# Performance work log

Hardware: AMD Instinct MI355X
Metric: run time of the kernel (lower is better)

Reference implementation:

```python
import jax, jax.numpy as jnp
import numpy as np

B, T, D = 1024, 20, 50          # batch sessions, seq len (hardcoded 20), emb dim (hardcoded 50)
S1S2 = 50 * 20                  # sample1 * sample2 friend nodes (GAT src)
DEG = 50                        # avg in-degree per dst node
E = B * DEG
NUM_USERS, NUM_ITEMS = 100000, 50000


def _lstm(x, W_ih, W_hh, b_ih, b_hh):
    """PyTorch-style LSTM (gate order i,f,g,o). x: [N,T,D] -> hs: [T,N,D]."""
    N = x.shape[0]
    h0 = jnp.zeros((N, x.shape[-1]), x.dtype)
    def step(carry, xt):
        h, c = carry
        gates = xt @ W_ih.T + h @ W_hh.T + b_ih + b_hh
        i, f, g, o = jnp.split(gates, 4, axis=-1)
        c = jax.nn.sigmoid(f) * c + jax.nn.sigmoid(i) * jnp.tanh(g)
        h = jax.nn.sigmoid(o) * jnp.tanh(c)
        return (h, c), h
    (_, _), hs = jax.lax.scan(step, (h0, h0), jnp.swapaxes(x, 0, 1))
    return hs


def _gat(feat_src, feat_dst, edge_src, edge_dst, fc_W, fc_b):
    """u_dot_v -> edge_softmax (per dst) -> u_mul_e_sum -> relu(fc)."""
    n_dst = feat_dst.shape[0]
    src_e = feat_src[edge_src]                           # [E, D] gather
    score = jnp.sum(src_e * feat_dst[edge_dst], axis=-1) # [E] u_dot_v
    m = jax.ops.segment_max(score, edge_dst, num_segments=n_dst)
    ex = jnp.exp(score - m[edge_dst])
    den = jax.ops.segment_sum(ex, edge_dst, num_segments=n_dst)
    w = ex / den[edge_dst]                               # edge_softmax
    agg = jax.ops.segment_sum(w[:, None] * src_e, edge_dst, num_segments=n_dst)
    return jax.nn.relu(agg @ fc_W.T + fc_b)


def setup_inputs() -> dict:
    key = jax.random.key(0)
    ks = jax.random.split(key, 16)
    input_session = jax.random.randint(ks[0], (B, T), 0, NUM_ITEMS, dtype=jnp.int32)
    support_nodes_layer1 = jax.random.randint(ks[1], (S1S2,), 0, NUM_USERS, dtype=jnp.int32)
    support_sessions_layer1 = jax.random.randint(ks[2], (S1S2, T), 0, NUM_ITEMS, dtype=jnp.int32)
    edge_src = jax.random.randint(ks[3], (E,), 0, S1S2, dtype=jnp.int32)
    edge_dst = jnp.repeat(jnp.arange(B, dtype=jnp.int32), DEG)  # every dst has DEG edges
    s = 0.05
    user_emb = jax.random.normal(ks[4], (NUM_USERS, D), jnp.float32) * s
    item_emb = (jax.random.normal(ks[5], (NUM_ITEMS, D), jnp.float32) * s).at[0].set(0.0)  # padding_idx=0
    W_ih = jax.random.normal(ks[6], (4 * D, D), jnp.float32) * s
    W_hh = jax.random.normal(ks[7], (4 * D, D), jnp.float32) * s
    b_ih = jax.random.normal(ks[8], (4 * D,), jnp.float32) * s
    b_hh = jax.random.normal(ks[9], (4 * D,), jnp.float32) * s
    W1 = jax.random.normal(ks[10], (D, 2 * D), jnp.float32) * s
    fc_W = jax.random.normal(ks[11], (D, D), jnp.float32) * s
    fc_b = jax.random.normal(ks[12], (D,), jnp.float32) * s
    W2 = jax.random.normal(ks[13], (D, 3 * D), jnp.float32) * s
    return {"input_session": input_session, "support_nodes_layer1": support_nodes_layer1,
            "support_sessions_layer1": support_sessions_layer1, "edge_src": edge_src,
            "edge_dst": edge_dst, "user_emb": user_emb, "item_emb": item_emb,
            "W_ih": W_ih, "W_hh": W_hh, "b_ih": b_ih, "b_hh": b_hh,
            "W1": W1, "fc_W": fc_W, "fc_b": fc_b, "W2": W2}


def reference(input_session, support_nodes_layer1, support_sessions_layer1, edge_src, edge_dst,
              user_emb, item_emb, W_ih, W_hh, b_ih, b_hh, W1, fc_W, fc_b, W2):
    # current-user short-term: LSTM over session item embeddings, take last hidden
    output = _lstm(item_emb[input_session], W_ih, W_hh, b_ih, b_hh)[-1]        # [B, D]
    # friends long-term (user emb) + short-term (LSTM over friend sessions, step 0 as in source)
    long_term1 = user_emb[support_nodes_layer1]                                 # [S1S2, D]
    short_term1 = _lstm(item_emb[support_sessions_layer1], W_ih, W_hh, b_ih, b_hh)[0]  # [S1S2, D]
    ls1 = jax.nn.relu(jnp.concatenate([long_term1, short_term1], axis=-1) @ W1.T)      # [S1S2, D]
    # GAT: gather -> per-dst edge softmax -> scatter weighted sum
    gat_out = _gat(ls1, output, edge_src, edge_dst, fc_W, fc_b)                 # [B, D]
    feat = jnp.concatenate([output, gat_out], axis=-1)                          # [B, 2D]
    sr = jnp.concatenate([output, feat], axis=-1) @ W2.T                        # [B, D]
    logits = sr @ item_emb[1:].T                                                # [B, NUM_ITEMS-1]
    return logits
```

## Files before the change

kernel.cpp:

```cpp
#include <hip/hip_runtime.h>
#include <math.h>

#define D 50
#define T 20
#define BATCH 1024
#define S1S2 1000
#define DEG 50
#define NITEMS 50000
#define NLOGITS 49999
#define KPAD 64
#define NIPAD 50048
#define LROW 520
#define CHUNKS 98
#define CHUNKS_PAD 104
#define PREP_BLKS ((NIPAD * (KPAD / 2) + 255) / 256)

using bf16x8 = __attribute__((ext_vector_type(8))) __bf16;
using f32x4  = __attribute__((ext_vector_type(4))) float;

__device__ __forceinline__ float sigf(float x) { return 1.0f / (1.0f + expf(-x)); }

__device__ __forceinline__ unsigned short f2bf(float f) {
    unsigned u = __builtin_bit_cast(unsigned, f);
    u = (u + 0x7FFFu + ((u >> 16) & 1u)) >> 16;
    return (unsigned short)u;
}

__global__ __launch_bounds__(256) void fused_front_kernel(
    const int* __restrict__ sess,
    const int* __restrict__ nodes,
    const int* __restrict__ fsess,
    const float* __restrict__ user_emb,
    const float* __restrict__ item_emb,
    const float* __restrict__ W_ih,
    const float* __restrict__ W_hh,
    const float* __restrict__ b_ih,
    const float* __restrict__ b_hh,
    const float* __restrict__ W1,
    float* __restrict__ out_h,
    float* __restrict__ ls1,
    unsigned* __restrict__ item_u)
{
    const int blk = blockIdx.x;
    const int t = threadIdx.x;

    if (blk < BATCH) {
        const int b = blk;
        __shared__ float x_s[D];
        __shared__ float h_s[D];
        __shared__ float g_s[4 * D];
        __shared__ int idx_s[T];

        if (t < T) idx_s[t] = sess[b * T + t];

        float wih[D], whh[D];
        float bias = 0.f;
        if (t < 4 * D) {
            #pragma unroll
            for (int k = 0; k < D; ++k) {
                wih[k] = W_ih[t * D + k];
                whh[k] = W_hh[t * D + k];
            }
            bias = b_ih[t] + b_hh[t];
        }
        float c = 0.f;
        if (t < D) h_s[t] = 0.f;
        __syncthreads();
        if (t < D) x_s[t] = item_emb[(size_t)idx_s[0] * D + t];
        __syncthreads();

        for (int step = 0; step < T; ++step) {
            float xn = 0.f;
            if (t < D && step + 1 < T)
                xn = item_emb[(size_t)idx_s[step + 1] * D + t];
            if (t < 4 * D) {
                float g = bias;
                #pragma unroll
                for (int k = 0; k < D; ++k)
                    g += wih[k] * x_s[k] + whh[k] * h_s[k];
                g_s[t] = g;
            }
            __syncthreads();
            if (t < D) {
                float ig = sigf(g_s[t]);
                float fg = sigf(g_s[D + t]);
                float gg = tanhf(g_s[2 * D + t]);
                float og = sigf(g_s[3 * D + t]);
                c = fg * c + ig * gg;
                h_s[t] = og * tanhf(c);
                if (step + 1 < T) x_s[t] = xn;
            }
            __syncthreads();
        }
        if (t < D) out_h[b * D + t] = h_s[t];
    } else if (blk < BATCH + S1S2) {
        const int s = blk - BATCH;
        __shared__ float fx_s[D];
        __shared__ float fh_s[D];
        __shared__ float fg_s[4 * D];

        if (t < D) fx_s[t] = item_emb[(size_t)fsess[s * T] * D + t];
        __syncthreads();
        if (t < 4 * D) {
            float g = b_ih[t] + b_hh[t];
            #pragma unroll
            for (int k = 0; k < D; ++k) g += W_ih[t * D + k] * fx_s[k];
            fg_s[t] = g;
        }
        __syncthreads();
        if (t < D) {
            float ig = sigf(fg_s[t]);
            float gg = tanhf(fg_s[2 * D + t]);
            float og = sigf(fg_s[3 * D + t]);
            float c1 = ig * gg;
            fh_s[t] = og * tanhf(c1);
        }
        __syncthreads();
        if (t < D) {
            const int node = nodes[s];
            const float* ue = user_emb + (size_t)node * D;
            const float* w1r = W1 + t * 2 * D;
            float acc = 0.f;
            #pragma unroll
            for (int k = 0; k < D; ++k) acc += ue[k] * w1r[k];
            #pragma unroll
            for (int k = 0; k < D; ++k) acc += fh_s[k] * w1r[D + k];
            ls1[s * D + t] = fmaxf(acc, 0.f);
        }
    } else {
        const int idx = (blk - BATCH - S1S2) * 256 + t;
        if (idx >= NIPAD * (KPAD / 2)) return;
        const int r = idx >> 5, c2 = idx & 31;
        const int c0 = c2 * 2, c1 = c0 + 1;
        float f0 = 0.f, f1 = 0.f;
        if (r < NLOGITS) {
            const float* row = item_emb + (size_t)(1 + r) * D;
            if (c0 < D) f0 = row[c0];
            if (c1 < D) f1 = row[c1];
        }
        item_u[idx] = (unsigned)f2bf(f0) | ((unsigned)f2bf(f1) << 16);
    }
}

__global__ __launch_bounds__(64) void gat_sr_kernel(
    const float* __restrict__ out_h,
    const float* __restrict__ ls1,
    const int* __restrict__ edge_src,
    const float* __restrict__ fc_W,
    const float* __restrict__ fc_b,
    const float* __restrict__ W2,
    unsigned* __restrict__ sr_u)
{
    const int b = blockIdx.x;
    const int l = threadIdx.x;
    __shared__ float q[D];
    __shared__ int srcs[DEG];
    __shared__ float w_s[DEG];
    __shared__ float a_s[D];
    __shared__ float g_s[D];
    __shared__ float srow_s[KPAD];

    srow_s[l] = 0.f;
    if (l < D) q[l] = out_h[b * D + l];
    if (l < DEG) srcs[l] = edge_src[b * DEG + l];
    __syncthreads();

    float sc = -INFINITY;
    if (l < DEG) {
        const float* row = ls1 + (size_t)srcs[l] * D;
        float s = 0.f;
        #pragma unroll
        for (int k = 0; k < D; ++k) s += row[k] * q[k];
        sc = s;
    }
    float m = sc;
    #pragma unroll
    for (int off = 32; off; off >>= 1) m = fmaxf(m, __shfl_xor(m, off));
    float ex = (l < DEG) ? expf(sc - m) : 0.f;
    float den = ex;
    #pragma unroll
    for (int off = 32; off; off >>= 1) den += __shfl_xor(den, off);
    if (l < DEG) w_s[l] = ex / den;
    __syncthreads();

    if (l < D) {
        float a = 0.f;
        #pragma unroll
        for (int j = 0; j < DEG; ++j) a += w_s[j] * ls1[(size_t)srcs[j] * D + l];
        a_s[l] = a;
    }
    __syncthreads();
    if (l < D) {
        float g = fc_b[l];
        #pragma unroll
        for (int k = 0; k < D; ++k) g += a_s[k] * fc_W[l * D + k];
        g_s[l] = fmaxf(g, 0.f);
    }
    __syncthreads();
    if (l < D) {
        const float* w2r = W2 + l * 3 * D;
        float v = 0.f;
        #pragma unroll
        for (int k = 0; k < D; ++k) v += q[k] * (w2r[k] + w2r[D + k]);
        #pragma unroll
        for (int k = 0; k < D; ++k) v += g_s[k] * w2r[2 * D + k];
        srow_s[l] = v;
    }
    __syncthreads();
    if (l < KPAD / 2) {
        unsigned u = (unsigned)f2bf(srow_s[2 * l]) |
                     ((unsigned)f2bf(srow_s[2 * l + 1]) << 16);
        sr_u[b * (KPAD / 2) + l] = u;
    }
}

__global__ __launch_bounds__(256) void logits_mfma_kernel(
    const unsigned short* __restrict__ sr_bf,
    const unsigned short* __restrict__ item_bf,
    float* __restrict__ out)
{
    const int n = blockIdx.x;
    const int slab = n / CHUNKS_PAD;
    const int j = n - slab * CHUNKS_PAD;
    const int chunk = (j & 7) * 13 + (j >> 3);
    if (chunk >= CHUNKS) return;

    const int t = threadIdx.x;
    const int lane = t & 63;
    const int wave = t >> 6;
    const int r16 = lane & 15;
    const int g   = lane >> 4;
    const int b0 = slab * 16;
    const int ibase = chunk * 512;
    const int i0w = ibase + wave * 128;

    __shared__ float ls[16 * LROW];

    const unsigned short* bp = sr_bf + (size_t)(b0 + r16) * KPAD + g * 8;
    bf16x8 bv0 = *(const bf16x8*)(bp);
    bf16x8 bv1 = *(const bf16x8*)(bp + 32);

    #pragma unroll
    for (int m = 0; m < 8; ++m) {
        int irow = i0w + m * 16 + r16;
        const unsigned short* ap =
            item_bf + (size_t)(irow < NIPAD ? irow : NIPAD - 1) * KPAD + g * 8;
        bf16x8 av0 = *(const bf16x8*)(ap);
        bf16x8 av1 = *(const bf16x8*)(ap + 32);
        f32x4 acc = {0.f, 0.f, 0.f, 0.f};
        acc = __builtin_amdgcn_mfma_f32_16x16x32_bf16(av0, bv0, acc, 0, 0, 0);
        acc = __builtin_amdgcn_mfma_f32_16x16x32_bf16(av1, bv1, acc, 0, 0, 0);
        *(f32x4*)&ls[r16 * LROW + wave * 128 + m * 16 + g * 4] = acc;
    }
    __syncthreads();

    #pragma unroll
    for (int pass = 0; pass < 4; ++pass) {
        const int row = wave * 4 + pass;
        float* orow = out + (size_t)(b0 + row) * NLOGITS + ibase;
        #pragma unroll
        for (int it2 = 0; it2 < 2; ++it2) {
            const int c = lane * 4 + it2 * 256;
            const int i = ibase + c;
            f32x4 v = *(const f32x4*)&ls[row * LROW + c];
            if (i + 3 < NLOGITS) {
                *(float4*)(orow + c) = make_float4(v[0], v[1], v[2], v[3]);
            } else {
                #pragma unroll
                for (int r = 0; r < 4; ++r)
                    if (i + r < NLOGITS) orow[c + r] = v[r];
            }
        }
    }
}

extern "C" void kernel_launch(void* const* d_in, const int* in_sizes, int n_in,
                              void* d_out, int out_size, void* d_ws, size_t ws_size,
                              hipStream_t stream) {
    const int*   sess      = (const int*)d_in[0];
    const int*   nodes     = (const int*)d_in[1];
    const int*   fsess     = (const int*)d_in[2];
    const int*   edge_src  = (const int*)d_in[3];
    const float* user_emb  = (const float*)d_in[5];
    const float* item_emb  = (const float*)d_in[6];
    const float* W_ih      = (const float*)d_in[7];
    const float* W_hh      = (const float*)d_in[8];
    const float* b_ih      = (const float*)d_in[9];
    const float* b_hh      = (const float*)d_in[10];
    const float* W1        = (const float*)d_in[11];
    const float* fc_W      = (const float*)d_in[12];
    const float* fc_b      = (const float*)d_in[13];
    const float* W2        = (const float*)d_in[14];
    float* out = (float*)d_out;

    char* ws = (char*)d_ws;
    float*    out_h  = (float*)(ws);
    float*    ls1    = (float*)(ws + 204800);
    unsigned* sr_u   = (unsigned*)(ws + 404800);
    unsigned* item_u = (unsigned*)(ws + 535872);

    hipLaunchKernelGGL(fused_front_kernel,
                       dim3(BATCH + S1S2 + PREP_BLKS), dim3(256), 0, stream,
                       sess, nodes, fsess, user_emb, item_emb,
                       W_ih, W_hh, b_ih, b_hh, W1, out_h, ls1, item_u);
    hipLaunchKernelGGL(gat_sr_kernel, dim3(BATCH), dim3(64), 0, stream,
                       out_h, ls1, edge_src, fc_W, fc_b, W2, sr_u);
    hipLaunchKernelGGL(logits_mfma_kernel,
                       dim3((BATCH / 16) * CHUNKS_PAD), dim3(256), 0, stream,
                       (const unsigned short*)sr_u, (const unsigned short*)item_u, out);
}
```

Baseline: 111.9 us.

## Retile logits GEMM to 64-batch by 64-item tiles with scalar stores

The logits kernel now gives each block a 64 batch rows by 64 items tile instead of 16 rows by 512 items. Each wave loads one item fragment and loops over four batch sub-tiles. The store phase writes one float per lane per row instead of float4 vectors. This changes the reuse balance between item rows and batch rows and the grid shape, and it pads the item count to 50176, which also grows the prep work. The trade is more blocks and narrower, possibly less efficient global stores against the ~200MB output write.

```diff
diff --git a/kernel.cpp b/kernel.cpp
--- a/kernel.cpp
+++ b/kernel.cpp
@@ -9,10 +9,11 @@
 #define NITEMS 50000
 #define NLOGITS 49999
 #define KPAD 64
-#define NIPAD 50048
-#define LROW 520
-#define CHUNKS 98
-#define CHUNKS_PAD 104
+#define SLAB 64
+#define CHW 64
+#define NCHN 784
+#define NIPAD (NCHN * CHW)
+#define LROWI 66
 #define PREP_BLKS ((NIPAD * (KPAD / 2) + 255) / 256)
 
 using bf16x8 = __attribute__((ext_vector_type(8))) __bf16;
@@ -220,57 +221,44 @@
     float* __restrict__ out)
 {
     const int n = blockIdx.x;
-    const int slab = n / CHUNKS_PAD;
-    const int j = n - slab * CHUNKS_PAD;
-    const int chunk = (j & 7) * 13 + (j >> 3);
-    if (chunk >= CHUNKS) return;
+    const int slab = n / NCHN;
+    const int j = n - slab * NCHN;
+    const int chunk = (j & 7) * 98 + (j >> 3);
 
     const int t = threadIdx.x;
     const int lane = t & 63;
     const int wave = t >> 6;
     const int r16 = lane & 15;
     const int g   = lane >> 4;
-    const int b0 = slab * 16;
-    const int ibase = chunk * 512;
-    const int i0w = ibase + wave * 128;
-
-    __shared__ float ls[16 * LROW];
-
-    const unsigned short* bp = sr_bf + (size_t)(b0 + r16) * KPAD + g * 8;
-    bf16x8 bv0 = *(const bf16x8*)(bp);
-    bf16x8 bv1 = *(const bf16x8*)(bp + 32);
-
-    #pragma unroll
-    for (int m = 0; m < 8; ++m) {
-        int irow = i0w + m * 16 + r16;
-        const unsigned short* ap =
-            item_bf + (size_t)(irow < NIPAD ? irow : NIPAD - 1) * KPAD + g * 8;
-        bf16x8 av0 = *(const bf16x8*)(ap);
-        bf16x8 av1 = *(const bf16x8*)(ap + 32);
+    const int b0 = slab * SLAB;
+    const int ibase = chunk * CHW;
+
+    __shared__ float ls[SLAB * LROWI];
+
+    const unsigned short* ap =
+        item_bf + (size_t)(ibase + wave * 16 + r16) * KPAD + g * 8;
+    bf16x8 av0 = *(const bf16x8*)(ap);
+    bf16x8 av1 = *(const bf16x8*)(ap + 32);
+
+    #pragma unroll
+    for (int bt = 0; bt < 4; ++bt) {
+        const unsigned short* bp = sr_bf + (size_t)(b0 + bt * 16 + r16) * KPAD + g * 8;
+        bf16x8 bv0 = *(const bf16x8*)(bp);
+        bf16x8 bv1 = *(const bf16x8*)(bp + 32);
         f32x4 acc = {0.f, 0.f, 0.f, 0.f};
         acc = __builtin_amdgcn_mfma_f32_16x16x32_bf16(av0, bv0, acc, 0, 0, 0);
         acc = __builtin_amdgcn_mfma_f32_16x16x32_bf16(av1, bv1, acc, 0, 0, 0);
-        *(f32x4*)&ls[r16 * LROW + wave * 128 + m * 16 + g * 4] = acc;
-    }
-    __syncthreads();
-
-    #pragma unroll
-    for (int pass = 0; pass < 4; ++pass) {
-        const int row = wave * 4 + pass;
-        float* orow = out + (size_t)(b0 + row) * NLOGITS + ibase;
-        #pragma unroll
-        for (int it2 = 0; it2 < 2; ++it2) {
-            const int c = lane * 4 + it2 * 256;
-            const int i = ibase + c;
-            f32x4 v = *(const f32x4*)&ls[row * LROW + c];
-            if (i + 3 < NLOGITS) {
-                *(float4*)(orow + c) = make_float4(v[0], v[1], v[2], v[3]);
-            } else {
-                #pragma unroll
-                for (int r = 0; r < 4; ++r)
-                    if (i + r < NLOGITS) orow[c + r] = v[r];
-            }
-        }
+        *(f32x4*)&ls[(bt * 16 + r16) * LROWI + wave * 16 + g * 4] = acc;
+    }
+    __syncthreads();
+
+    const int i = ibase + lane;
+    const bool ok = i < NLOGITS;
+    #pragma unroll
+    for (int p = 0; p < 16; ++p) {
+        const int brow = wave * 16 + p;
+        float v = ls[brow * LROWI + lane];
+        if (ok) out[(size_t)(b0 + brow) * NLOGITS + i] = v;
     }
 }
 
@@ -306,6 +294,6 @@
     hipLaunchKernelGGL(gat_sr_kernel, dim3(BATCH), dim3(64), 0, stream,
                        out_h, ls1, edge_src, fc_W, fc_b, W2, sr_u);
     hipLaunchKernelGGL(logits_mfma_kernel,
-                       dim3((BATCH / 16) * CHUNKS_PAD), dim3(256), 0, stream,
+                       dim3((BATCH / SLAB) * NCHN), dim3(256), 0, stream,
                        (const unsigned short*)sr_u, (const unsigned short*)item_u, out);
 }
```

Result: slower. 115.5 us (+3.2%).
